# Kernel optimization log

Measured on AMD Instinct MI355X. Metric: run time of the kernel, lower is better.

The kernel has to match this reference:

```python
import jax, jax.numpy as jnp
import numpy as np

N, IN_DIM, HID, HEADS, OUT_DIM = 4096, 512, 128, 4, 64
ALPHA = 0.2
NEG_INF = -9e15  # matches torch's -9000000000000000.0 fill


def _gat_layer(adj_mask, h, W, a, concat):
    # h: [N, Fin], W: [Fin, Fout], a: [2*Fout, 1]
    Wh = h @ W                                   # [N, Fout]
    f_out = W.shape[1]
    Wh1 = Wh @ a[:f_out]                         # [N, 1]
    Wh2 = Wh @ a[f_out:]                         # [N, 1]
    e = jax.nn.leaky_relu(Wh1 + Wh2.T, ALPHA)    # [N, N] broadcast scores
    e = jnp.where(adj_mask, e, NEG_INF)
    att = jax.nn.softmax(e, axis=1)              # masked row softmax
    out = att @ Wh                               # [N, Fout] aggregate
    return jax.nn.elu(out) if concat else out


def setup_inputs() -> dict:
    key = jax.random.key(0)
    k = jax.random.split(key, 6)
    g = jax.random.randint(k[0], (N, N), 0, 2, dtype=jnp.int32)
    inputs = jax.random.normal(k[1], (N, IN_DIM), dtype=jnp.float32)
    # xavier-uniform-like scales
    s1 = np.sqrt(6.0 / (IN_DIM + HID)) * 1.414
    sa1 = np.sqrt(6.0 / (2 * HID + 1)) * 1.414
    s2 = np.sqrt(6.0 / (HID * HEADS + OUT_DIM)) * 1.414
    sa2 = np.sqrt(6.0 / (2 * OUT_DIM + 1)) * 1.414
    W1 = jax.random.uniform(k[2], (HEADS, IN_DIM, HID), jnp.float32, -s1, s1)
    a1 = jax.random.uniform(k[3], (HEADS, 2 * HID, 1), jnp.float32, -sa1, sa1)
    W2 = jax.random.uniform(k[4], (HID * HEADS, OUT_DIM), jnp.float32, -s2, s2)
    a2 = jax.random.uniform(k[5], (2 * OUT_DIM, 1), jnp.float32, -sa2, sa2)
    return {"g": g, "inputs": inputs, "W1": W1, "a1": a1, "W2": W2, "a2": a2}


def reference(g, inputs, W1, a1, W2, a2):
    adj_mask = g > 0                                              # [N, N] bool
    # layer 1: HEADS parallel heads, concat=True (elu), then concat on features
    heads_out = jax.vmap(lambda W, a: _gat_layer(adj_mask, inputs, W, a, True))(W1, a1)
    h = jnp.transpose(heads_out, (1, 0, 2)).reshape(N, HEADS * HID)  # [N, H*HID]
    # output attention layer, concat=False (no elu)
    return _gat_layer(adj_mask, h, W2, a2, False)                 # [N, OUT_DIM]
```

## Files before the change

kernel.cpp:

```cpp
#include <hip/hip_runtime.h>
#include <hip/hip_bf16.h>
#include <stdint.h>

#define NN 4096
#define KD 512

typedef __attribute__((ext_vector_type(8))) short short8;
typedef __attribute__((ext_vector_type(4))) float f32x4;

__device__ __forceinline__ float lrelu(float x) { return fmaxf(x, 0.2f * x); }

__device__ __forceinline__ unsigned short f2bf(float f) {
    uint32_t u = __float_as_uint(f);
    u += 0x7fff + ((u >> 16) & 1);
    return (unsigned short)(u >> 16);
}

__device__ __forceinline__ void glds16(const void* g, void* l) {
    __builtin_amdgcn_global_load_lds(
        (const __attribute__((address_space(1))) uint32_t*)g,
        (__attribute__((address_space(3))) uint32_t*)l, 16, 0, 0);
}

__global__ void k_bitmask(const int* __restrict__ g, uint64_t* __restrict__ bm) {
    int wave = threadIdx.x >> 6;
    int lane = threadIdx.x & 63;
    int row = blockIdx.x * 4 + wave;
    const int* grow = g + (size_t)row * NN;
    for (int w = 0; w < 64; ++w) {
        int v = grow[w * 64 + lane];
        unsigned long long m = __ballot(v > 0);
        if (lane == 0) bm[(size_t)row * 64 + w] = m;
    }
}

__global__ void k_cast(const float* __restrict__ x, unsigned short* __restrict__ y, int n4) {
    int i = blockIdx.x * 256 + threadIdx.x;
    if (i < n4) {
        float4 v = ((const float4*)x)[i];
        uint2 o;
        o.x = (uint32_t)f2bf(v.x) | ((uint32_t)f2bf(v.y) << 16);
        o.y = (uint32_t)f2bf(v.z) | ((uint32_t)f2bf(v.w) << 16);
        ((uint2*)y)[i] = o;
    }
}

__global__ __launch_bounds__(256)
void k_tc(const float* __restrict__ src, unsigned short* __restrict__ dst, int R, int C) {
    __shared__ float tile[64][65];
    int b = blockIdx.z;
    int r0 = blockIdx.x * 64, c0 = blockIdx.y * 64;
    src += (size_t)b * R * C;
    dst += (size_t)b * C * R;
    int t = threadIdx.x;
    #pragma unroll
    for (int s = 0; s < 16; ++s) {
        int idx = t + s * 256;
        int r = idx >> 6, c = idx & 63;
        tile[r][c] = src[(size_t)(r0 + r) * C + c0 + c];
    }
    __syncthreads();
    #pragma unroll
    for (int s = 0; s < 16; ++s) {
        int idx = t + s * 256;
        int r = idx >> 6, c = idx & 63;
        dst[(size_t)(c0 + r) * R + r0 + c] = f2bf(tile[c][r]);
    }
}

template <int F>
__global__ __launch_bounds__(512)
void k_gemm_fused(const unsigned short* __restrict__ Abf, const unsigned short* __restrict__ WT,
                  const float* __restrict__ avec,
                  unsigned short* __restrict__ WhT, float* __restrict__ s1g,
                  float* __restrict__ s2g, unsigned int* __restrict__ smaxKey) {
    constexpr int BM = 32, BK = 64;
    constexpr int NCF = F / 64;
    __shared__ unsigned short a_lds[2][BM * BK];
    __shared__ unsigned short b_lds[2][F * BK];
    __shared__ unsigned short t_lds[F * 40];
    __shared__ float sred[BM][2];
    int t = threadIdx.x, lane = t & 63, w = t >> 6;
    int h = blockIdx.y;
    int i0 = blockIdx.x * BM;
    const unsigned short* WTh = WT + (size_t)h * F * KD;
    int r0 = (w >> 2) * 16, c0 = (w & 3) * (F / 4);
    int krow = lane & 15, kgrp = lane >> 4;
    if (t < BM) { sred[t][0] = 0.f; sred[t][1] = 0.f; }
    f32x4 acc[NCF];
    #pragma unroll
    for (int cf = 0; cf < NCF; ++cf) acc[cf] = (f32x4){0.f, 0.f, 0.f, 0.f};

    auto stage = [&](int buf, int kt) {
        int k0 = kt * BK;
        if (w < 4) {
            int c = w * 64 + lane;
            int row = c >> 3, slot = c & 7;
            glds16(Abf + (size_t)(i0 + row) * KD + k0 + ((slot ^ (row & 7)) * 8),
                   &a_lds[buf][(w * 64) * 8]);
        }
        #pragma unroll
        for (int s = 0; s < F / 64; ++s) {
            int c = w * F + s * 64 + lane;
            int row = c >> 3, slot = c & 7;
            glds16(WTh + (size_t)row * KD + k0 + ((slot ^ (row & 7)) * 8),
                   &b_lds[buf][(w * F + s * 64) * 8]);
        }
    };

    stage(0, 0);
    __syncthreads();
    int cur = 0;
    for (int kt = 0; kt < KD / BK; ++kt) {
        int nxt = cur ^ 1;
        if (kt + 1 < KD / BK) stage(nxt, kt + 1);
        #pragma unroll
        for (int ks = 0; ks < 2; ++ks) {
            int koff = ks * 32 + kgrp * 8;
            int arow = r0 + krow;
            short8 av = *(const short8*)((const char*)&a_lds[cur][arow * BK] +
                                         ((koff * 2) ^ ((arow & 7) << 4)));
            #pragma unroll
            for (int cf = 0; cf < NCF; ++cf) {
                int brow = c0 + cf * 16 + krow;
                short8 bv = *(const short8*)((const char*)&b_lds[cur][brow * BK] +
                                             ((koff * 2) ^ ((brow & 7) << 4)));
                acc[cf] = __builtin_amdgcn_mfma_f32_16x16x32_bf16(av, bv, acc[cf], 0, 0, 0);
            }
        }
        __syncthreads();
        cur = nxt;
    }
    float p1[4] = {0.f, 0.f, 0.f, 0.f}, p2[4] = {0.f, 0.f, 0.f, 0.f};
    const float* ah = avec + (size_t)h * 2 * F;
    #pragma unroll
    for (int cf = 0; cf < NCF; ++cf) {
        int col = c0 + cf * 16 + krow;
        float aw1 = ah[col], aw2 = ah[F + col];
        #pragma unroll
        for (int r = 0; r < 4; ++r) {
            int row = r0 + kgrp * 4 + r;
            t_lds[col * 40 + row] = f2bf(acc[cf][r]);
            p1[r] += acc[cf][r] * aw1;
            p2[r] += acc[cf][r] * aw2;
        }
    }
    #pragma unroll
    for (int d = 1; d < 16; d <<= 1) {
        #pragma unroll
        for (int r = 0; r < 4; ++r) { p1[r] += __shfl_xor(p1[r], d); p2[r] += __shfl_xor(p2[r], d); }
    }
    if (krow == 0) {
        #pragma unroll
        for (int r = 0; r < 4; ++r) {
            int row = r0 + kgrp * 4 + r;
            atomicAdd(&sred[row][0], p1[r]);
            atomicAdd(&sred[row][1], p2[r]);
        }
    }
    __syncthreads();
    {
        int col = t >> 2, seg = (t & 3) * 8;
        if (col < F) {
            uint4 v = *(const uint4*)&t_lds[col * 40 + seg];
            *(uint4*)&WhT[((size_t)h * F + col) * NN + i0 + seg] = v;
        }
    }
    if (t < BM) {
        s1g[(size_t)h * NN + i0 + t] = sred[t][0];
        s2g[(size_t)h * NN + i0 + t] = sred[t][1];
    }
    if (w == 0) {
        float v = (t < BM) ? sred[t][1] : -3.4e38f;
        #pragma unroll
        for (int d = 1; d < 64; d <<= 1) v = fmaxf(v, __shfl_xor(v, d));
        if (lane == 0) {
            uint32_t b = __float_as_uint(v);
            uint32_t key = (b & 0x80000000u) ? ~b : (b | 0x80000000u);
            atomicMax(smaxKey + h, key);
        }
    }
}

template <int F, int NW>
__global__ __launch_bounds__(NW * 64, 2)
void k_agg3(const unsigned short* __restrict__ WhT, const float* __restrict__ s1v,
            const float* __restrict__ s2v, const unsigned int* __restrict__ smaxKey,
            const unsigned char* __restrict__ bmb,
            float* __restrict__ pnum, float* __restrict__ pden, int njt, int nh) {
    constexpr int TI = (NW / 2) * 32, TJ = 64;
    constexpr int NB = F / 16;
    constexpr int CH_W = F * 8 / NW;
    __shared__ unsigned short whT_lds[3][F * TJ];
    __shared__ float den_sh[2][TI];
    int t = threadIdx.x, l = t & 63, w = t >> 6;
    int h = blockIdx.y, js = blockIdx.z;
    int i0 = blockIdx.x * TI;
    int rg = w >> 1, jh = w & 1;
    int r0 = rg * 32;
    const unsigned short* WhTh = WhT + (size_t)h * F * NN;
    const float* s2h = s2v + (size_t)h * NN;
    unsigned int kk = smaxKey[h];
    float smax = __uint_as_float((kk & 0x80000000u) ? (kk ^ 0x80000000u) : ~kk);
    int rowA = i0 + r0 + (l & 15);
    int rowB = rowA + 16;
    float s1A = s1v[(size_t)h * NN + rowA];
    float s1B = s1v[(size_t)h * NN + rowB];
    float miA = lrelu(s1A + smax), miB = lrelu(s1B + smax);
    int joff = jh * 32 + (l >> 4) * 8;
    int jsbase = js * njt;
    const unsigned char* bmbA = bmb + (size_t)rowA * 512;
    const unsigned char* bmbB = bmb + (size_t)rowB * 512;

    f32x4 acc[2][NB];
    #pragma unroll
    for (int m = 0; m < 2; ++m)
        #pragma unroll
        for (int b = 0; b < NB; ++b) acc[m][b] = (f32x4){0.f, 0.f, 0.f, 0.f};
    float denA = 0.f, denB = 0.f;

    struct SD { float4 q0, q1; unsigned int mA, mB; };
    struct PA { short8 a, b; };

    auto loadSD = [&](int jt) {
        SD s;
        int j0 = (jsbase + jt) * TJ;
        s.q0 = *(const float4*)&s2h[j0 + joff];
        s.q1 = *(const float4*)&s2h[j0 + joff + 4];
        int wb = (jsbase + jt) * 8 + jh * 4 + (l >> 4);
        s.mA = bmbA[wb];
        s.mB = bmbB[wb];
        return s;
    };

    auto computeP = [&](const SD& s) {
        float q[8] = {s.q0.x, s.q0.y, s.q0.z, s.q0.w, s.q1.x, s.q1.y, s.q1.z, s.q1.w};
        union { unsigned short u[8]; short8 v; } ua, ub;
        #pragma unroll
        for (int u = 0; u < 8; ++u) {
            float eA = s1A + q[u];
            eA = fmaxf(eA, 0.2f * eA);
            float pA = ((s.mA >> u) & 1u) ? __expf(eA - miA) : 0.f;
            unsigned short hA = f2bf(pA);
            ua.u[u] = hA;
            denA += __uint_as_float((uint32_t)hA << 16);
            float eB = s1B + q[u];
            eB = fmaxf(eB, 0.2f * eB);
            float pB = ((s.mB >> u) & 1u) ? __expf(eB - miB) : 0.f;
            unsigned short hB = f2bf(pB);
            ub.u[u] = hB;
            denB += __uint_as_float((uint32_t)hB << 16);
        }
        PA p; p.a = ua.v; p.b = ub.v;
        return p;
    };

    auto stage = [&](int buf, int jt) {
        int j0 = (jsbase + jt) * TJ;
        #pragma unroll
        for (int s = 0; s < CH_W / 64; ++s) {
            int c = w * CH_W + s * 64 + l;
            int row = c >> 3, slot = c & 7;
            glds16(WhTh + (size_t)row * NN + j0 + ((slot ^ (row & 7)) * 8),
                   &whT_lds[buf][(w * CH_W + s * 64) * 8]);
        }
    };

    auto domfma = [&](int buf, const PA& pa) {
        #pragma unroll
        for (int b = 0; b < NB; ++b) {
            int brow = b * 16 + (l & 15);
            short8 bv = *(const short8*)((const char*)&whT_lds[buf][brow * TJ] +
                         ((jh * 64 + (l >> 4) * 16) ^ ((brow & 7) << 4)));
            acc[0][b] = __builtin_amdgcn_mfma_f32_16x16x32_bf16(pa.a, bv, acc[0][b], 0, 0, 0);
            acc[1][b] = __builtin_amdgcn_mfma_f32_16x16x32_bf16(pa.b, bv, acc[1][b], 0, 0, 0);
        }
    };

    SD sd_cur = loadSD(0);
    stage(0, 0);
    SD sd_nxt;
    if (njt > 1) sd_nxt = loadSD(1);
    PA pa_cur = computeP(sd_cur);
    __syncthreads();
    int cur = 0, nx1 = 1;
    for (int jt = 0; jt < njt; ++jt) {
        bool more = jt + 1 < njt;
        if (more) stage(nx1, jt + 1);
        SD sd2;
        if (jt + 2 < njt) sd2 = loadSD(jt + 2);
        PA pa_n;
        if (more) pa_n = computeP(sd_nxt);
        __syncthreads();
        domfma(cur, pa_cur);
        pa_cur = pa_n;
        sd_nxt = sd2;
        cur = nx1;
        nx1 = nx1 + 1 == 3 ? 0 : nx1 + 1;
    }

    denA += __shfl_xor(denA, 16); denA += __shfl_xor(denA, 32);
    denB += __shfl_xor(denB, 16); denB += __shfl_xor(denB, 32);
    if (l < 16) {
        den_sh[jh][r0 + l] = denA;
        den_sh[jh][r0 + 16 + l] = denB;
    }
    __syncthreads();

    float* xch = (float*)whT_lds;
    float* pnumS = pnum + ((size_t)(js * nh + h) * NN + i0) * F;
    #pragma unroll
    for (int m = 0; m < 2; ++m) {
        if (jh == 1) {
            #pragma unroll
            for (int b = 0; b < NB; ++b) {
                int col = b * 16 + (l & 15);
                #pragma unroll
                for (int r = 0; r < 4; ++r)
                    xch[(rg * 16 + (l >> 4) * 4 + r) * F + col] = acc[m][b][r];
            }
        }
        __syncthreads();
        if (jh == 0) {
            #pragma unroll
            for (int b = 0; b < NB; ++b) {
                int col = b * 16 + (l & 15);
                #pragma unroll
                for (int r = 0; r < 4; ++r) {
                    int lrow = rg * 16 + (l >> 4) * 4 + r;
                    int row = r0 + m * 16 + (l >> 4) * 4 + r;
                    pnumS[(size_t)row * F + col] = acc[m][b][r] + xch[(size_t)lrow * F + col];
                }
            }
        }
        __syncthreads();
    }
    if (t < TI) pden[(size_t)(js * nh + h) * NN + i0 + t] = den_sh[0][t] + den_sh[1][t];
}

__global__ void k_reduce1(const float* __restrict__ pnum, const float* __restrict__ pden,
                          unsigned short* __restrict__ hbuf) {
    int idx = blockIdx.x * 256 + threadIdx.x;
    int i = idx >> 7;
    int c4 = idx & 127;
    int hh = c4 >> 5, f4 = c4 & 31;
    float4 a = *(const float4*)&pnum[((size_t)hh * NN + i) * 128 + f4 * 4];
    float4 b = *(const float4*)&pnum[((size_t)(4 + hh) * NN + i) * 128 + f4 * 4];
    float den = pden[(size_t)hh * NN + i] + pden[(size_t)(4 + hh) * NN + i];
    float inv = 1.f / den;
    float v[4] = {(a.x + b.x) * inv, (a.y + b.y) * inv, (a.z + b.z) * inv, (a.w + b.w) * inv};
    uint2 o;
    unsigned short e[4];
    #pragma unroll
    for (int u = 0; u < 4; ++u) {
        float x = v[u];
        x = x > 0.f ? x : expm1f(x);
        e[u] = f2bf(x);
    }
    o.x = (uint32_t)e[0] | ((uint32_t)e[1] << 16);
    o.y = (uint32_t)e[2] | ((uint32_t)e[3] << 16);
    *(uint2*)&hbuf[(size_t)i * 512 + c4 * 4] = o;
}

__global__ void k_reduce2(const float* __restrict__ pnum, const float* __restrict__ pden,
                          float* __restrict__ out) {
    int idx = blockIdx.x * 256 + threadIdx.x;
    int i = idx >> 4;
    int f4 = (idx & 15) * 4;
    float4 s = {0.f, 0.f, 0.f, 0.f};
    float den = 0.f;
    #pragma unroll
    for (int js = 0; js < 8; ++js) {
        float4 v = *(const float4*)&pnum[((size_t)js * NN + i) * 64 + f4];
        s.x += v.x; s.y += v.y; s.z += v.z; s.w += v.w;
        den += pden[(size_t)js * NN + i];
    }
    float inv = 1.f / den;
    s.x *= inv; s.y *= inv; s.z *= inv; s.w *= inv;
    *(float4*)&out[(size_t)i * 64 + f4] = s;
}

extern "C" void kernel_launch(void* const* d_in, const int* in_sizes, int n_in,
                              void* d_out, int out_size, void* d_ws, size_t ws_size,
                              hipStream_t stream) {
    const int*   g      = (const int*)d_in[0];
    const float* inputs = (const float*)d_in[1];
    const float* W1     = (const float*)d_in[2];
    const float* a1     = (const float*)d_in[3];
    const float* W2     = (const float*)d_in[4];
    const float* a2     = (const float*)d_in[5];
    float* out = (float*)d_out;
    char* ws = (char*)d_ws;

    size_t off = 0;
    uint64_t* bm   = (uint64_t*)(ws + off); off += (size_t)NN * 64 * 8;
    unsigned short* Xbf  = (unsigned short*)(ws + off); off += (size_t)NN * KD * 2;
    unsigned short* W1T  = (unsigned short*)(ws + off); off += (size_t)4 * 128 * KD * 2;
    unsigned short* W2T  = (unsigned short*)(ws + off); off += (size_t)64 * KD * 2;
    unsigned short* WhT1 = (unsigned short*)(ws + off); off += (size_t)4 * 128 * NN * 2;
    unsigned short* WhT2 = (unsigned short*)(ws + off); off += (size_t)64 * NN * 2;
    unsigned short* hbuf = (unsigned short*)(ws + off); off += (size_t)NN * KD * 2;
    float* s1_1    = (float*)(ws + off);    off += (size_t)4 * NN * 4;
    float* s2_1    = (float*)(ws + off);    off += (size_t)4 * NN * 4;
    float* s1_2    = (float*)(ws + off);    off += (size_t)NN * 4;
    float* s2_2    = (float*)(ws + off);    off += (size_t)NN * 4;
    unsigned int* keys = (unsigned int*)(ws + off); off += 256;
    float* pnum    = (float*)(ws + off);    off += (size_t)8 * NN * 128 * 4;
    float* pden    = (float*)(ws + off);    off += (size_t)8 * NN * 4;
    float* pnum2 = pnum;
    float* pden2 = pden;

    hipMemsetAsync(keys, 0, 32, stream);
    k_bitmask<<<NN / 4, 256, 0, stream>>>(g, bm);
    k_cast<<<(NN * KD / 4 + 255) / 256, 256, 0, stream>>>(inputs, Xbf, NN * KD / 4);
    k_tc<<<dim3(KD / 64, 2, 4), 256, 0, stream>>>(W1, W1T, KD, 128);
    k_tc<<<dim3(KD / 64, 1, 1), 256, 0, stream>>>(W2, W2T, KD, 64);
    k_gemm_fused<128><<<dim3(NN / 32, 4), 512, 0, stream>>>(Xbf, W1T, a1, WhT1, s1_1, s2_1, keys);
    k_agg3<128, 8><<<dim3(NN / 128, 4, 2), 512, 0, stream>>>(
        WhT1, s1_1, s2_1, keys, (const unsigned char*)bm, pnum, pden, NN / 64 / 2, 4);
    k_reduce1<<<NN * 128 / 256, 256, 0, stream>>>(pnum, pden, hbuf);
    k_gemm_fused<64><<<dim3(NN / 32, 1), 512, 0, stream>>>(hbuf, W2T, a2, WhT2, s1_2, s2_2, keys + 4);
    k_agg3<64, 4><<<dim3(NN / 64, 1, 8), 256, 0, stream>>>(
        WhT2, s1_2, s2_2, keys + 4, (const unsigned char*)bm, pnum2, pden2, NN / 64 / 8, 1);
    k_reduce2<<<NN * 16 / 256, 256, 0, stream>>>(pnum2, pden2, out);
}
```

Before: 130.6 us.

## Split aggregation j-tile across four warp groups and double block size

Generalizes the attention aggregation kernel so NJH warps share each 32-row group, each covering a different 32-column slice of the j-tile. The j-tile grows to 128 and blocks double to 1024/512 threads, and partial sums from the extra slices are reduced through LDS at the end. The aim is to halve the number of j-iterations and barriers per block and raise the warps available to hide latency. In exchange, LDS staging buffers double in size, the cross-warp reduction grows, and the raised launch-bounds occupancy target constrains registers.

```diff
diff --git a/kernel.cpp b/kernel.cpp
--- a/kernel.cpp
+++ b/kernel.cpp
@@ -182,21 +182,22 @@
     }
 }
 
-template <int F, int NW>
-__global__ __launch_bounds__(NW * 64, 2)
+template <int F, int NW, int NJH>
+__global__ __launch_bounds__(NW * 64, 4)
 void k_agg3(const unsigned short* __restrict__ WhT, const float* __restrict__ s1v,
             const float* __restrict__ s2v, const unsigned int* __restrict__ smaxKey,
             const unsigned char* __restrict__ bmb,
             float* __restrict__ pnum, float* __restrict__ pden, int njt, int nh) {
-    constexpr int TI = (NW / 2) * 32, TJ = 64;
+    constexpr int TI = (NW / NJH) * 32, TJ = NJH * 32;
     constexpr int NB = F / 16;
-    constexpr int CH_W = F * 8 / NW;
+    constexpr int CPR = TJ / 8;
+    constexpr int CH_W = F * CPR / NW;
     __shared__ unsigned short whT_lds[3][F * TJ];
-    __shared__ float den_sh[2][TI];
+    __shared__ float den_sh[NJH][TI];
     int t = threadIdx.x, l = t & 63, w = t >> 6;
     int h = blockIdx.y, js = blockIdx.z;
     int i0 = blockIdx.x * TI;
-    int rg = w >> 1, jh = w & 1;
+    int rg = w / NJH, jh = w % NJH;
     int r0 = rg * 32;
     const unsigned short* WhTh = WhT + (size_t)h * F * NN;
     const float* s2h = s2v + (size_t)h * NN;
@@ -227,7 +228,7 @@
         int j0 = (jsbase + jt) * TJ;
         s.q0 = *(const float4*)&s2h[j0 + joff];
         s.q1 = *(const float4*)&s2h[j0 + joff + 4];
-        int wb = (jsbase + jt) * 8 + jh * 4 + (l >> 4);
+        int wb = (jsbase + jt) * CPR + jh * 4 + (l >> 4);
         s.mA = bmbA[wb];
         s.mB = bmbB[wb];
         return s;
@@ -260,7 +261,7 @@
         #pragma unroll
         for (int s = 0; s < CH_W / 64; ++s) {
             int c = w * CH_W + s * 64 + l;
-            int row = c >> 3, slot = c & 7;
+            int row = c / CPR, slot = c % CPR;
             glds16(WhTh + (size_t)row * NN + j0 + ((slot ^ (row & 7)) * 8),
                    &whT_lds[buf][(w * CH_W + s * 64) * 8]);
         }
@@ -307,17 +308,19 @@
     }
     __syncthreads();
 
+    constexpr int XROWS = TI / 2;
     float* xch = (float*)whT_lds;
     float* pnumS = pnum + ((size_t)(js * nh + h) * NN + i0) * F;
     #pragma unroll
     for (int m = 0; m < 2; ++m) {
-        if (jh == 1) {
+        if (jh > 0) {
+            float* sl = xch + (size_t)(jh - 1) * XROWS * F;
             #pragma unroll
             for (int b = 0; b < NB; ++b) {
                 int col = b * 16 + (l & 15);
                 #pragma unroll
                 for (int r = 0; r < 4; ++r)
-                    xch[(rg * 16 + (l >> 4) * 4 + r) * F + col] = acc[m][b][r];
+                    sl[(rg * 16 + (l >> 4) * 4 + r) * F + col] = acc[m][b][r];
             }
         }
         __syncthreads();
@@ -329,13 +332,22 @@
                 for (int r = 0; r < 4; ++r) {
                     int lrow = rg * 16 + (l >> 4) * 4 + r;
                     int row = r0 + m * 16 + (l >> 4) * 4 + r;
-                    pnumS[(size_t)row * F + col] = acc[m][b][r] + xch[(size_t)lrow * F + col];
+                    float v = acc[m][b][r];
+                    #pragma unroll
+                    for (int sX = 1; sX < NJH; ++sX)
+                        v += xch[((size_t)(sX - 1) * XROWS + lrow) * F + col];
+                    pnumS[(size_t)row * F + col] = v;
                 }
             }
         }
         __syncthreads();
     }
-    if (t < TI) pden[(size_t)(js * nh + h) * NN + i0 + t] = den_sh[0][t] + den_sh[1][t];
+    if (t < TI) {
+        float d = den_sh[0][t];
+        #pragma unroll
+        for (int sX = 1; sX < NJH; ++sX) d += den_sh[sX][t];
+        pden[(size_t)(js * nh + h) * NN + i0 + t] = d;
+    }
 }
 
 __global__ void k_reduce1(const float* __restrict__ pnum, const float* __restrict__ pden,
@@ -416,11 +428,11 @@
     k_tc<<<dim3(KD / 64, 2, 4), 256, 0, stream>>>(W1, W1T, KD, 128);
     k_tc<<<dim3(KD / 64, 1, 1), 256, 0, stream>>>(W2, W2T, KD, 64);
     k_gemm_fused<128><<<dim3(NN / 32, 4), 512, 0, stream>>>(Xbf, W1T, a1, WhT1, s1_1, s2_1, keys);
-    k_agg3<128, 8><<<dim3(NN / 128, 4, 2), 512, 0, stream>>>(
-        WhT1, s1_1, s2_1, keys, (const unsigned char*)bm, pnum, pden, NN / 64 / 2, 4);
+    k_agg3<128, 16, 4><<<dim3(NN / 128, 4, 2), 1024, 0, stream>>>(
+        WhT1, s1_1, s2_1, keys, (const unsigned char*)bm, pnum, pden, NN / 128 / 2, 4);
     k_reduce1<<<NN * 128 / 256, 256, 0, stream>>>(pnum, pden, hbuf);
     k_gemm_fused<64><<<dim3(NN / 32, 1), 512, 0, stream>>>(hbuf, W2T, a2, WhT2, s1_2, s2_2, keys + 4);
-    k_agg3<64, 4><<<dim3(NN / 64, 1, 8), 256, 0, stream>>>(
-        WhT2, s1_2, s2_2, keys + 4, (const unsigned char*)bm, pnum2, pden2, NN / 64 / 8, 1);
+    k_agg3<64, 8, 4><<<dim3(NN / 64, 1, 8), 512, 0, stream>>>(
+        WhT2, s1_2, s2_2, keys + 4, (const unsigned char*)bm, pnum2, pden2, NN / 128 / 8, 1);
     k_reduce2<<<NN * 16 / 256, 256, 0, stream>>>(pnum2, pden2, out);
 }
```

New measurement: 128.7 us. Within noise of the previous version (-1.5%).
